# Performance work log

Measured on AMD Instinct MI355X. Metric: run time of the kernel, lower is better.

## Reference

```python
import jax, jax.numpy as jnp
import numpy as np

B, C, H, W, P, D, NH = 16, 3, 512, 512, 16, 128, 4
GH, GW = H // P, W // P
NP_ = GH * GW            # 1024 total patches
PD = C * P * P           # 768 patch dim
NV = NP_ // 4            # 256 visible tokens (mask_ratio = 0.75)
ENC_L, DEC_L = 6, 2
FF = 4 * D

def layer_norm(x, w, b, eps=1e-5):
    m = jnp.mean(x, -1, keepdims=True)
    v = jnp.mean((x - m) ** 2, -1, keepdims=True)
    return (x - m) * jax.lax.rsqrt(v + eps) * w + b

def mha(x, qkv_w, qkv_b, out_w, out_b):
    Bq, S, Dm = x.shape
    hd = Dm // NH
    q, k, v = jnp.split(x @ qkv_w.T + qkv_b, 3, axis=-1)
    sh = lambda t: t.reshape(Bq, S, NH, hd).transpose(0, 2, 1, 3)
    q, k, v = sh(q), sh(k), sh(v)
    scale = jnp.asarray(1.0 / np.sqrt(hd), x.dtype)
    att = jax.nn.softmax(jnp.einsum('bhqd,bhkd->bhqk', q, k) * scale, axis=-1)
    o = jnp.einsum('bhqk,bhkd->bhqd', att, v).transpose(0, 2, 1, 3).reshape(Bq, S, Dm)
    return o @ out_w.T + out_b

def stack(x, qkv_w, qkv_b, out_w, out_b, ln1_w, ln1_b, ff1_w, ff1_b, ff2_w, ff2_b, ln2_w, ln2_b):
    # post-norm nn.TransformerEncoderLayer, eval mode (dropout off), exact gelu
    for i in range(qkv_w.shape[0]):
        x = layer_norm(x + mha(x, qkv_w[i], qkv_b[i], out_w[i], out_b[i]), ln1_w[i], ln1_b[i])
        h = jax.nn.gelu(x @ ff1_w[i].T + ff1_b[i], approximate=False) @ ff2_w[i].T + ff2_b[i]
        x = layer_norm(x + h, ln2_w[i], ln2_b[i])
    return x

def setup_inputs():
    key = jax.random.key(0)
    ks = iter(jax.random.split(key, 64))
    f = lambda *s: jax.random.normal(next(ks), s, jnp.float32) * 0.02
    inp = {
        'x': jax.random.normal(next(ks), (B, C, H, W), jnp.float32),
        'vis_idx': jax.vmap(lambda k: jax.random.permutation(k, NP_))(jax.random.split(next(ks), B))[:, :NV].astype(jnp.int32),
        'w_patch': f(D, PD), 'b_patch': jnp.zeros((D,), jnp.float32),
        'mask_token': f(1, D), 'pos_embed': f(1, NP_, D),
        'w_recon': f(PD, D), 'b_recon': jnp.zeros((PD,), jnp.float32),
    }
    for pre, L in (('enc', ENC_L), ('dec', DEC_L)):
        inp[pre + '_qkv_w'] = f(L, 3 * D, D)
        inp[pre + '_qkv_b'] = jnp.zeros((L, 3 * D), jnp.float32)
        inp[pre + '_out_w'] = f(L, D, D)
        inp[pre + '_out_b'] = jnp.zeros((L, D), jnp.float32)
        inp[pre + '_ln1_w'] = jnp.ones((L, D), jnp.float32)
        inp[pre + '_ln1_b'] = jnp.zeros((L, D), jnp.float32)
        inp[pre + '_ff1_w'] = f(L, FF, D)
        inp[pre + '_ff1_b'] = jnp.zeros((L, FF), jnp.float32)
        inp[pre + '_ff2_w'] = f(L, D, FF)
        inp[pre + '_ff2_b'] = jnp.zeros((L, D), jnp.float32)
        inp[pre + '_ln2_w'] = jnp.ones((L, D), jnp.float32)
        inp[pre + '_ln2_b'] = jnp.zeros((L, D), jnp.float32)
    return inp

def reference(x, vis_idx, w_patch, b_patch, mask_token, pos_embed, w_recon, b_recon,
              enc_qkv_w, enc_qkv_b, enc_out_w, enc_out_b, enc_ln1_w, enc_ln1_b,
              enc_ff1_w, enc_ff1_b, enc_ff2_w, enc_ff2_b, enc_ln2_w, enc_ln2_b,
              dec_qkv_w, dec_qkv_b, dec_out_w, dec_out_b, dec_ln1_w, dec_ln1_b,
              dec_ff1_w, dec_ff1_b, dec_ff2_w, dec_ff2_b, dec_ln2_w, dec_ln2_b):
    # patchify: matches nn.Unfold(kernel=stride=P) channel-major patch layout
    patches = x.reshape(B, C, GH, P, GW, P).transpose(0, 2, 4, 1, 3, 5).reshape(B, NP_, PD)
    tok = patches @ w_patch.T + b_patch                    # [B, NP, D]
    bidx = jnp.arange(B)[:, None]
    vis = tok[bidx, vis_idx]                               # [B, NV, D] packed visible tokens
    enc = stack(vis, enc_qkv_w, enc_qkv_b, enc_out_w, enc_out_b, enc_ln1_w, enc_ln1_b,
                enc_ff1_w, enc_ff1_b, enc_ff2_w, enc_ff2_b, enc_ln2_w, enc_ln2_b)
    # mask_token everywhere, scatter encoded tokens back to their positions
    full = jnp.broadcast_to(mask_token, (B, NP_, D)).at[bidx, vis_idx].set(enc)
    full = full + pos_embed
    dec = stack(full, dec_qkv_w, dec_qkv_b, dec_out_w, dec_out_b, dec_ln1_w, dec_ln1_b,
                dec_ff1_w, dec_ff1_b, dec_ff2_w, dec_ff2_b, dec_ln2_w, dec_ln2_b)
    rec = dec @ w_recon.T + b_recon                        # [B, NP, PD]
    # unpatchify: [B,GH,GW,C,P,P] -> permute(0,3,1,4,2,5) -> [B,C,H,W]
    img = rec.reshape(B, GH, GW, C, P, P).transpose(0, 3, 1, 4, 2, 5).reshape(B, C, H, W)
    return img
```

## Files before the change

kernel.cpp:

```cpp
#include <hip/hip_runtime.h>
#include <math.h>

typedef unsigned short ushort_t;
typedef __attribute__((ext_vector_type(8))) short bf16x8;
typedef __attribute__((ext_vector_type(4))) float f32x4;
typedef __attribute__((ext_vector_type(16))) float f32x16;
typedef __attribute__((ext_vector_type(2))) unsigned uint2v;

__device__ __forceinline__ ushort_t f2bf(float f){
  union{float f; unsigned u;} v; v.f = f;
  unsigned r = v.u + 0x7FFFu + ((v.u >> 16) & 1u);
  return (ushort_t)(r >> 16);
}
__device__ __forceinline__ float bf2f(ushort_t h){
  union{unsigned u; float f;} v; v.u = ((unsigned)h) << 16; return v.f;
}
__device__ __forceinline__ float erf_fast(float x){
  float ax = fabsf(x);
  float t = 1.f / fmaf(0.3275911f, ax, 1.f);
  float y = t*fmaf(t, fmaf(t, fmaf(t, fmaf(t, 1.061405429f, -1.453152027f),
            1.421413741f), -0.284496736f), 0.254829592f);
  float r = 1.f - y * __expf(-ax*ax);
  return copysignf(r, x);
}
__device__ __forceinline__ float gelu_fast(float v){
  return 0.5f * v * (1.f + erf_fast(v * 0.70710678118654752f));
}
#define GLD16(gp, lp) __builtin_amdgcn_global_load_lds( \
    (const __attribute__((address_space(1))) void*)(gp), \
    (__attribute__((address_space(3))) void*)(lp), 16, 0, 0)

static __device__ __forceinline__ f32x4 mfma16(bf16x8 a, bf16x8 b, f32x4 c){
  return __builtin_amdgcn_mfma_f32_16x16x32_bf16(a, b, c, 0, 0, 0);
}
static __device__ __forceinline__ f32x16 mfma32(bf16x8 a, bf16x8 b, f32x16 c){
  return __builtin_amdgcn_mfma_f32_32x32x16_bf16(a, b, c, 0, 0, 0);
}

template<int BT, int MI, int SRC, int EPI>
__global__ __launch_bounds__(256) void mfma_gemm(
    const ushort_t* __restrict__ A, const ushort_t* __restrict__ W,
    const float* __restrict__ bias, void* __restrict__ Cout,
    int M, int N, int K, ushort_t* __restrict__ vT, int slog, float qs)
{
  __shared__ ushort_t smem[BT*64 + BT*64];
  ushort_t* Al = smem;
  ushort_t* Wl = smem + BT*64;
  const int tid = threadIdx.x;
  const int lane = tid & 63, w = tid >> 6;
  const int wr = w >> 1, wc = w & 1;
  const int g = lane >> 4, lq = lane & 15;
  const int m0 = blockIdx.y * BT, n0 = blockIdx.x * BT;

  const f32x4 zf = {0.f, 0.f, 0.f, 0.f};
  f32x4 acc[MI][MI];
#pragma unroll
  for (int i = 0; i < MI; ++i)
#pragma unroll
    for (int j = 0; j < MI; ++j) acc[i][j] = zf;

  float bv[MI];
#pragma unroll
  for (int ni = 0; ni < MI; ++ni) bv[ni] = bias[n0 + wc*(BT/2) + ni*16 + lq];

  const int KT = K >> 6;
  for (int kt = 0; kt < KT; ++kt) {
    if (kt) __syncthreads();
    const int k0 = kt << 6;
#pragma unroll
    for (int i = 0; i < BT/32; ++i) {
      int chunk = i*256 + tid;
      int row = chunk >> 3, c = chunk & 7;
      int kk = k0 + ((c ^ (row & 7)) << 3);
      const ushort_t* src;
      if (SRC == 0) {
        src = A + (size_t)(m0 + row) * K + kk;
      } else {
        int gm = m0 + row;
        int bb = gm >> 10, pp = gm & 1023, gh = pp >> 5, gw = pp & 31;
        int ci = kk >> 8, rem = kk & 255, py = rem >> 4, px = rem & 15;
        src = A + ((size_t)((bb*3 + ci)*512 + gh*16 + py) * 512 + gw*16 + px);
      }
      GLD16(src, (char*)Al + chunk*16);
    }
#pragma unroll
    for (int i = 0; i < BT/32; ++i) {
      int chunk = i*256 + tid;
      int row = chunk >> 3, c = chunk & 7;
      int kk = k0 + ((c ^ (row & 7)) << 3);
      GLD16(W + (size_t)(n0 + row) * K + kk, (char*)Wl + chunk*16);
    }
    __syncthreads();
#pragma unroll
    for (int ks = 0; ks < 2; ++ks) {
      bf16x8 af[MI], bfr[MI];
#pragma unroll
      for (int mi = 0; mi < MI; ++mi) {
        int row = wr*(BT/2) + mi*16 + lq;
        int c = (ks*4 + g) ^ (row & 7);
        af[mi] = *(const bf16x8*)((const char*)Al + row*128 + c*16);
      }
#pragma unroll
      for (int ni = 0; ni < MI; ++ni) {
        int row = wc*(BT/2) + ni*16 + lq;
        int c = (ks*4 + g) ^ (row & 7);
        bfr[ni] = *(const bf16x8*)((const char*)Wl + row*128 + c*16);
      }
#pragma unroll
      for (int mi = 0; mi < MI; ++mi)
#pragma unroll
        for (int ni = 0; ni < MI; ++ni)
          acc[mi][ni] = mfma16(af[mi], bfr[ni], acc[mi][ni]);
    }
  }

  if (EPI == 3 && n0 >= 256) {
    const int Sm1 = (1 << slog) - 1;
#pragma unroll
    for (int mi = 0; mi < MI; ++mi) {
      int gm0 = m0 + wr*(BT/2) + mi*16 + g*4;
      int bb = gm0 >> slog, s0 = gm0 & Sm1;
#pragma unroll
      for (int ni = 0; ni < MI; ++ni) {
        int n = n0 + wc*(BT/2) + ni*16 + lq;
        int vcol = n - 256, hh = vcol >> 5, dd = vcol & 31;
        unsigned pw0 = ((unsigned)f2bf(acc[mi][ni][0] + bv[ni])) |
                       (((unsigned)f2bf(acc[mi][ni][1] + bv[ni])) << 16);
        unsigned pw1 = ((unsigned)f2bf(acc[mi][ni][2] + bv[ni])) |
                       (((unsigned)f2bf(acc[mi][ni][3] + bv[ni])) << 16);
        uint2 pk; pk.x = pw0; pk.y = pw1;
        *(uint2*)(vT + (((size_t)(bb*4 + hh)*32 + dd) << slog) + s0) = pk;
      }
    }
    return;
  }

  if (EPI == 2) {
    float* img = (float*)Cout;
#pragma unroll
    for (int mi = 0; mi < MI; ++mi) {
#pragma unroll
      for (int r = 0; r < 4; ++r) {
        int gm = m0 + wr*(BT/2) + mi*16 + g*4 + r;
        int bb = gm >> 10, pp = gm & 1023, gh = pp >> 5, gw = pp & 31;
#pragma unroll
        for (int ni = 0; ni < MI; ++ni) {
          int n = n0 + wc*(BT/2) + ni*16 + lq;
          int ci = n >> 8, rem = n & 255, py = rem >> 4, px = rem & 15;
          img[(size_t)((bb*3 + ci)*512 + gh*16 + py)*512 + gw*16 + px] =
              acc[mi][ni][r] + bv[ni];
        }
      }
    }
  } else {
    const float cs = (EPI == 3 && n0 < 128) ? qs : 1.0f;
    __syncthreads();
    constexpr int CPR = BT/8;
#pragma unroll
    for (int mi = 0; mi < MI; ++mi)
#pragma unroll
      for (int ni = 0; ni < MI; ++ni)
#pragma unroll
        for (int r = 0; r < 4; ++r) {
          int row = wr*(BT/2) + mi*16 + g*4 + r;
          int col = wc*(BT/2) + ni*16 + lq;
          float v = acc[mi][ni][r] + bv[ni];
          if (EPI == 3) v *= cs;
          int cc = (col >> 3) ^ (row & (CPR-1));
          smem[row*BT + cc*8 + (col & 7)] = f2bf(v);
        }
    __syncthreads();
    ushort_t* Co = (ushort_t*)Cout;
#pragma unroll
    for (int i = 0; i < BT*BT/2048; ++i) {
      int chunk = i*256 + tid;
      int row = chunk / CPR, cc = chunk % CPR;
      int c = cc ^ (row & (CPR-1));
      bf16x8 v = *(const bf16x8*)((const char*)smem + chunk*16);
      *(bf16x8*)(Co + (size_t)(m0+row)*N + n0 + c*8) = v;
    }
  }
}

template<int MI2, int QKV>
__global__ __launch_bounds__(512, 4) void mega8(
    const ushort_t* __restrict__ Ao, const ushort_t* __restrict__ Wo,
    const float* __restrict__ bo, ushort_t* __restrict__ X,
    const float* __restrict__ l1w, const float* __restrict__ l1b,
    const ushort_t* __restrict__ W1, const float* __restrict__ b1,
    const ushort_t* __restrict__ W2, const float* __restrict__ b2,
    const float* __restrict__ l2w, const float* __restrict__ l2b,
    const ushort_t* __restrict__ Wq, const float* __restrict__ bq,
    ushort_t* __restrict__ qkvb, ushort_t* __restrict__ vT,
    int slog, float qs)
{
  constexpr int BM = MI2 * 16;
  constexpr int TB = BM * 128;
  __shared__ __align__(16) ushort_t Xl[2*BM*64];
  __shared__ __align__(16) ushort_t Hl[8*BM*64];
  __shared__ __align__(16) float red[2][BM][8];
  const int tid = threadIdx.x, lane = tid & 63, w = tid >> 6;
  const int g = lane >> 4, lq = lane & 15;
  const int m0 = blockIdx.x * BM;
  const int col0 = w*16 + lq;
  const f32x4 zf = {0.f,0.f,0.f,0.f};

  f32x4 acc[MI2];
#pragma unroll
  for (int mi = 0; mi < MI2; ++mi) acc[mi] = zf;
  {
    bf16x8 a1[MI2][4], bo8[4];
#pragma unroll
    for (int mi = 0; mi < MI2; ++mi)
#pragma unroll
      for (int kf = 0; kf < 4; ++kf)
        a1[mi][kf] = *(const bf16x8*)(Ao + (size_t)(m0 + mi*16 + lq)*128 + kf*32 + g*8);
#pragma unroll
    for (int kf = 0; kf < 4; ++kf)
      bo8[kf] = *(const bf16x8*)(Wo + (size_t)col0*128 + kf*32 + g*8);
#pragma unroll
    for (int kf = 0; kf < 4; ++kf)
#pragma unroll
      for (int mi = 0; mi < MI2; ++mi)
        acc[mi] = mfma16(a1[mi][kf], bo8[kf], acc[mi]);
  }

  float xp[MI2][4];
  {
    const float bv = bo[col0], lwv = l1w[col0], lbv = l1b[col0];
#pragma unroll
    for (int mi = 0; mi < MI2; ++mi)
#pragma unroll
      for (int r = 0; r < 4; ++r) {
        int row = m0 + mi*16 + g*4 + r;
        float v = acc[mi][r] + bv + bf2f(X[(size_t)row*128 + col0]);
        xp[mi][r] = v;
        float s = v, q = v*v;
        s += __shfl_xor(s,1); s += __shfl_xor(s,2); s += __shfl_xor(s,4); s += __shfl_xor(s,8);
        q += __shfl_xor(q,1); q += __shfl_xor(q,2); q += __shfl_xor(q,4); q += __shfl_xor(q,8);
        if (lq == 0) { red[0][mi*16+g*4+r][w] = s; red[1][mi*16+g*4+r][w] = q; }
      }
    __syncthreads();
#pragma unroll
    for (int mi = 0; mi < MI2; ++mi)
#pragma unroll
      for (int r = 0; r < 4; ++r) {
        int rl = mi*16 + g*4 + r;
        float4 s0 = *(const float4*)&red[0][rl][0], s1 = *(const float4*)&red[0][rl][4];
        float4 q0 = *(const float4*)&red[1][rl][0], q1 = *(const float4*)&red[1][rl][4];
        float s = s0.x+s0.y+s0.z+s0.w + s1.x+s1.y+s1.z+s1.w;
        float q = q0.x+q0.y+q0.z+q0.w + q1.x+q1.y+q1.z+q1.w;
        float mean = s * 0.0078125f;
        float var = q * 0.0078125f - mean*mean;
        float rstd = rsqrtf(var + 1e-5f);
        float val = (xp[mi][r]-mean)*rstd*lwv + lbv;
        xp[mi][r] = val;
        int kt = col0 >> 6, c8 = (col0 & 63) >> 3, he = col0 & 7;
        *(ushort_t*)((char*)Xl + kt*TB + rl*128 + ((c8 ^ (rl & 7)) << 4) + he*2) = f2bf(val);
      }
  }
  __syncthreads();

  bf16x8 a2[MI2][4];
#pragma unroll
  for (int mi = 0; mi < MI2; ++mi)
#pragma unroll
    for (int kf = 0; kf < 4; ++kf) {
      int kt = kf >> 1, row = mi*16 + lq;
      int c = ((kf & 1)*4 + g) ^ (row & 7);
      a2[mi][kf] = *(const bf16x8*)((const char*)Xl + kt*TB + row*128 + c*16);
    }

#pragma unroll
  for (int hp = 0; hp < 4; ++hp) {
    const int hid = hp*128 + col0;
    bf16x8 b18[4];
#pragma unroll
    for (int kf = 0; kf < 4; ++kf)
      b18[kf] = *(const bf16x8*)(W1 + (size_t)hid*128 + kf*32 + g*8);
    f32x4 acc1[MI2];
#pragma unroll
    for (int mi = 0; mi < MI2; ++mi) acc1[mi] = zf;
#pragma unroll
    for (int kf = 0; kf < 4; ++kf)
#pragma unroll
      for (int mi = 0; mi < MI2; ++mi)
        acc1[mi] = mfma16(a2[mi][kf], b18[kf], acc1[mi]);
    const float bb = b1[hid];
    const int hkt = hid >> 6, hc8 = (hid & 63) >> 3, he = hid & 7;
#pragma unroll
    for (int mi = 0; mi < MI2; ++mi)
#pragma unroll
      for (int r = 0; r < 4; ++r) {
        int mrow = mi*16 + g*4 + r;
        float hv = gelu_fast(acc1[mi][r] + bb);
        *(ushort_t*)((char*)Hl + hkt*TB + mrow*128 + ((hc8 ^ (mrow & 7)) << 4) + he*2) = f2bf(hv);
      }
  }
  __syncthreads();

  f32x4 acc2[MI2];
#pragma unroll
  for (int mi = 0; mi < MI2; ++mi) acc2[mi] = zf;
#pragma unroll
  for (int kf = 0; kf < 16; ++kf) {
    int kt = kf >> 1;
    bf16x8 af[MI2], bfr;
#pragma unroll
    for (int mi = 0; mi < MI2; ++mi) {
      int row = mi*16 + lq;
      int c = ((kf & 1)*4 + g) ^ (row & 7);
      af[mi] = *(const bf16x8*)((const char*)Hl + kt*TB + row*128 + c*16);
    }
    bfr = *(const bf16x8*)(W2 + (size_t)col0*512 + kf*32 + g*8);
#pragma unroll
    for (int mi = 0; mi < MI2; ++mi)
      acc2[mi] = mfma16(af[mi], bfr, acc2[mi]);
  }

  {
    const float bv = b2[col0], lwv = l2w[col0], lbv = l2b[col0];
#pragma unroll
    for (int mi = 0; mi < MI2; ++mi)
#pragma unroll
      for (int r = 0; r < 4; ++r) {
        float v = acc2[mi][r] + bv + xp[mi][r];
        xp[mi][r] = v;
        float s = v, q = v*v;
        s += __shfl_xor(s,1); s += __shfl_xor(s,2); s += __shfl_xor(s,4); s += __shfl_xor(s,8);
        q += __shfl_xor(q,1); q += __shfl_xor(q,2); q += __shfl_xor(q,4); q += __shfl_xor(q,8);
        if (lq == 0) { red[0][mi*16+g*4+r][w] = s; red[1][mi*16+g*4+r][w] = q; }
      }
    __syncthreads();
#pragma unroll
    for (int mi = 0; mi < MI2; ++mi)
#pragma unroll
      for (int r = 0; r < 4; ++r) {
        int rl = mi*16 + g*4 + r;
        float4 s0 = *(const float4*)&red[0][rl][0], s1 = *(const float4*)&red[0][rl][4];
        float4 q0 = *(const float4*)&red[1][rl][0], q1 = *(const float4*)&red[1][rl][4];
        float s = s0.x+s0.y+s0.z+s0.w + s1.x+s1.y+s1.z+s1.w;
        float q = q0.x+q0.y+q0.z+q0.w + q1.x+q1.y+q1.z+q1.w;
        float mean = s * 0.0078125f;
        float var = q * 0.0078125f - mean*mean;
        float rstd = rsqrtf(var + 1e-5f);
        float val = (xp[mi][r]-mean)*rstd*lwv + lbv;
        ushort_t hv = f2bf(val);
        X[(size_t)(m0+rl)*128 + col0] = hv;
        if (QKV) {
          int kt = col0 >> 6, c8 = (col0 & 63) >> 3, he = col0 & 7;
          *(ushort_t*)((char*)Xl + kt*TB + rl*128 + ((c8 ^ (rl & 7)) << 4) + he*2) = hv;
        }
      }
  }

  if (QKV) {
    __syncthreads();
    bf16x8 a3[MI2][4];
#pragma unroll
    for (int mi = 0; mi < MI2; ++mi)
#pragma unroll
      for (int kf = 0; kf < 4; ++kf) {
        int kt = kf >> 1, row = mi*16 + lq;
        int c = ((kf & 1)*4 + g) ^ (row & 7);
        a3[mi][kf] = *(const bf16x8*)((const char*)Xl + kt*TB + row*128 + c*16);
      }
    const int Sm1 = (1 << slog) - 1;
#pragma unroll
    for (int pp = 0; pp < 3; ++pp) {
      const int colq = pp*128 + col0;
      bf16x8 bq8[4];
#pragma unroll
      for (int kf = 0; kf < 4; ++kf)
        bq8[kf] = *(const bf16x8*)(Wq + (size_t)colq*128 + kf*32 + g*8);
      f32x4 aq[MI2];
#pragma unroll
      for (int mi = 0; mi < MI2; ++mi) aq[mi] = zf;
#pragma unroll
      for (int kf = 0; kf < 4; ++kf)
#pragma unroll
        for (int mi = 0; mi < MI2; ++mi)
          aq[mi] = mfma16(a3[mi][kf], bq8[kf], aq[mi]);
      const float bias = bq[colq];
      if (pp < 2) {
        const float sc = (pp == 0) ? qs : 1.f;
#pragma unroll
        for (int mi = 0; mi < MI2; ++mi)
#pragma unroll
          for (int r = 0; r < 4; ++r) {
            int row = m0 + mi*16 + g*4 + r;
            qkvb[(size_t)row*384 + colq] = f2bf((aq[mi][r] + bias)*sc);
          }
      } else {
        const int hh = col0 >> 5, dd = col0 & 31;
#pragma unroll
        for (int mi = 0; mi < MI2; ++mi) {
          int gm0 = m0 + mi*16 + g*4;
          int bb = gm0 >> slog, s0 = gm0 & Sm1;
          unsigned pw0 = ((unsigned)f2bf(aq[mi][0] + bias)) |
                         (((unsigned)f2bf(aq[mi][1] + bias)) << 16);
          unsigned pw1 = ((unsigned)f2bf(aq[mi][2] + bias)) |
                         (((unsigned)f2bf(aq[mi][3] + bias)) << 16);
          uint2 pk; pk.x = pw0; pk.y = pw1;
          *(uint2*)(vT + (((size_t)(bb*4 + hh)*32 + dd) << slog) + s0) = pk;
        }
      }
    }
  }
}

template<int S, int NTW>
__global__ __launch_bounds__(256) void attn32s(
    const ushort_t* __restrict__ qkv, const ushort_t* __restrict__ vTg,
    ushort_t* __restrict__ o)
{
  __shared__ __align__(16) char smem[32768];
  const int tid = threadIdx.x, lane = tid & 63, w = tid >> 6;
  const int hi = lane >> 5, lq = lane & 31;
  constexpr int QB = S/32;
  constexpr int NBLK = QB*64;
  int lin = blockIdx.x;
  int nid = (lin & 7)*(NBLK/8) + (lin >> 3);
  int bx = nid % QB, bh = nid / QB;
  int h = bh & 3, b = bh >> 2;
  const int q0 = bx*32;

  bf16x8 bq0 = *(const bf16x8*)(qkv + (size_t)(b*S + q0 + lq)*384 + h*32 + hi*8);
  bf16x8 bq1 = *(const bf16x8*)(qkv + (size_t)(b*S + q0 + lq)*384 + h*32 + 16 + hi*8);

  f32x16 O;
#pragma unroll
  for (int i = 0; i < 16; ++i) O[i] = 0.f;
  const f32x16 z16 = O;
  float l = 0.f;

  char* Kb = smem + w*8192;
  char* Vb = Kb + 4096;

  auto stageK = [&](int j0, int ci){
    int k = ci >> 2, cp = ci & 3, c = cp ^ (k & 3);
    GLD16(qkv + (size_t)(b*S + j0 + k)*384 + 128 + h*32 + c*8, Kb + ci*16);
  };
  auto stageV = [&](int j0, int ci){
    int d = ci >> 3, cp = ci & 7, c = cp ^ (d & 7);
    GLD16(vTg + (size_t)(bh*32 + d)*S + j0 + c*8, Vb + ci*16);
  };
  auto sm_pack = [&](const f32x16& stv, unsigned* wd){
    float p[16];
#pragma unroll
    for (int r = 0; r < 16; ++r) { p[r] = __expf(stv[r]); l += p[r]; }
#pragma unroll
    for (int i = 0; i < 8; ++i) {
      unsigned u0 = __float_as_uint(p[2*i])   + 0x8000u;
      unsigned u1 = __float_as_uint(p[2*i+1]) + 0x8000u;
      wd[i] = (u0 >> 16) | (u1 & 0xFFFF0000u);
    }
  };
  auto pvstep = [&](unsigned* wd, int mt){
    uint2v s02 = __builtin_amdgcn_permlane32_swap(wd[0], wd[2], false, false);
    uint2v s13 = __builtin_amdgcn_permlane32_swap(wd[1], wd[3], false, false);
    uint2v s46 = __builtin_amdgcn_permlane32_swap(wd[4], wd[6], false, false);
    uint2v s57 = __builtin_amdgcn_permlane32_swap(wd[5], wd[7], false, false);
    union { unsigned u[4]; bf16x8 v; } pa0, pa1;
    pa0.u[0] = s02[0]; pa0.u[1] = s13[0]; pa0.u[2] = s02[1]; pa0.u[3] = s13[1];
    pa1.u[0] = s46[0]; pa1.u[1] = s57[0]; pa1.u[2] = s46[1]; pa1.u[3] = s57[1];
    int d = lq;
    bf16x8 v0 = *(const bf16x8*)(Vb + d*128 + (((mt*4 + hi)     ^ (d & 7)) << 4));
    bf16x8 v1 = *(const bf16x8*)(Vb + d*128 + (((mt*4 + 2 + hi) ^ (d & 7)) << 4));
    O = mfma32(pa0.v, v0, O);
    O = mfma32(pa1.v, v1, O);
  };
  auto computeTile = [&](){
    const int k0 = lq, k1 = 32 + lq;
    bf16x8 a00 = *(const bf16x8*)(Kb + k0*64 + (((hi)     ^ (k0 & 3)) << 4));
    bf16x8 a01 = *(const bf16x8*)(Kb + k0*64 + (((2 + hi) ^ (k0 & 3)) << 4));
    f32x16 st0 = mfma32(a00, bq0, z16);
    st0 = mfma32(a01, bq1, st0);
    bf16x8 a10 = *(const bf16x8*)(Kb + k1*64 + (((hi)     ^ (k1 & 3)) << 4));
    bf16x8 a11 = *(const bf16x8*)(Kb + k1*64 + (((2 + hi) ^ (k1 & 3)) << 4));
    f32x16 st1 = mfma32(a10, bq0, z16);
    st1 = mfma32(a11, bq1, st1);
    unsigned wd0[8], wd1[8];
    sm_pack(st0, wd0);
    sm_pack(st1, wd1);
    pvstep(wd0, 0);
    pvstep(wd1, 1);
  };

#pragma unroll
  for (int i = 0; i < NTW; ++i) {
    const int j0 = (w + 4*i)*64;
#pragma unroll
    for (int c = 0; c < 4; ++c) stageK(j0, c*64 + lane);
#pragma unroll
    for (int c = 0; c < 4; ++c) stageV(j0, c*64 + lane);
    asm volatile("s_waitcnt vmcnt(0)" ::: "memory");
    __builtin_amdgcn_sched_barrier(0);
    computeTile();
    asm volatile("" ::: "memory");
  }

  float lw = l + __shfl_xor(l, 32);
  __syncthreads();
  float* F = (float*)smem;
#pragma unroll
  for (int r = 0; r < 16; ++r) F[(w*16 + r)*64 + lane] = O[r];
  if (hi == 0) F[4096 + w*32 + lq] = lw;
  __syncthreads();
  if (w == 0) {
    float lt = F[4096 + lq] + F[4096 + 32 + lq] + F[4096 + 64 + lq] + F[4096 + 96 + lq];
    float linv = 1.f / lt;
#pragma unroll
    for (int r = 0; r < 16; ++r) {
      float s = F[r*64 + lane] + F[(16 + r)*64 + lane] +
                F[(32 + r)*64 + lane] + F[(48 + r)*64 + lane];
      int qr = (r & 3) + 8*(r >> 2) + 4*hi;
      float li = __shfl(linv, qr);
      o[(size_t)(b*S + q0 + qr)*128 + h*32 + lq] = f2bf(s*li);
    }
  }
}

struct CastArgs {
  const float* src[11];
  ushort_t* dst[11];
  int start[11];
};
__global__ __launch_bounds__(256) void cast_all(CastArgs a, int total8){
  int i = blockIdx.x*256 + threadIdx.x;
  if (i >= total8) return;
  int s = 0;
#pragma unroll
  for (int k = 1; k < 11; ++k) if (i >= a.start[k]) s = k;
  int off = (i - a.start[s]) * 8;
  const float* sp = a.src[s] + off;
  float4 f0 = *(const float4*)sp;
  float4 f1 = *(const float4*)(sp + 4);
  bf16x8 r;
  r[0]=(short)f2bf(f0.x); r[1]=(short)f2bf(f0.y); r[2]=(short)f2bf(f0.z); r[3]=(short)f2bf(f0.w);
  r[4]=(short)f2bf(f1.x); r[5]=(short)f2bf(f1.y); r[6]=(short)f2bf(f1.z); r[7]=(short)f2bf(f1.w);
  *(bf16x8*)(a.dst[s] + off) = r;
}

__global__ __launch_bounds__(256) void gather_k(const ushort_t* __restrict__ tok,
    const int* __restrict__ vis, ushort_t* __restrict__ xe){
  int i = blockIdx.x*256 + threadIdx.x;
  int r = i >> 4, e = (i & 15)*8;
  int b = r >> 8;
  int p = vis[r];
  *(bf16x8*)(xe + (size_t)r*128 + e) = *(const bf16x8*)(tok + ((size_t)b*1024 + p)*128 + e);
}

__global__ __launch_bounds__(256) void fill_k(const float* __restrict__ mask_tok,
    const float* __restrict__ pos, ushort_t* __restrict__ full){
  int i = blockIdx.x*256 + threadIdx.x;
  int off0 = i*8;
  int d = off0 & 127;
  int p = (off0 >> 7) & 1023;
  float4 m0 = *(const float4*)(mask_tok + d);
  float4 m1 = *(const float4*)(mask_tok + d + 4);
  const float* pp = pos + (size_t)p*128 + d;
  float4 p0 = *(const float4*)pp, p1 = *(const float4*)(pp + 4);
  bf16x8 r;
  r[0]=(short)f2bf(m0.x+p0.x); r[1]=(short)f2bf(m0.y+p0.y);
  r[2]=(short)f2bf(m0.z+p0.z); r[3]=(short)f2bf(m0.w+p0.w);
  r[4]=(short)f2bf(m1.x+p1.x); r[5]=(short)f2bf(m1.y+p1.y);
  r[6]=(short)f2bf(m1.z+p1.z); r[7]=(short)f2bf(m1.w+p1.w);
  *(bf16x8*)(full + off0) = r;
}

__global__ __launch_bounds__(256) void scatter_k(const ushort_t* __restrict__ enc,
    const int* __restrict__ vis, const float* __restrict__ pos, ushort_t* __restrict__ full){
  int i = blockIdx.x*256 + threadIdx.x;
  int r = i >> 4, e = (i & 15)*8;
  int b = r >> 8;
  int p = vis[r];
  bf16x8 ev = *(const bf16x8*)(enc + (size_t)r*128 + e);
  const float* pp = pos + (size_t)p*128 + e;
  float4 p0 = *(const float4*)pp, p1 = *(const float4*)(pp + 4);
  bf16x8 out;
  out[0]=(short)f2bf(bf2f((ushort_t)ev[0]) + p0.x);
  out[1]=(short)f2bf(bf2f((ushort_t)ev[1]) + p0.y);
  out[2]=(short)f2bf(bf2f((ushort_t)ev[2]) + p0.z);
  out[3]=(short)f2bf(bf2f((ushort_t)ev[3]) + p0.w);
  out[4]=(short)f2bf(bf2f((ushort_t)ev[4]) + p1.x);
  out[5]=(short)f2bf(bf2f((ushort_t)ev[5]) + p1.y);
  out[6]=(short)f2bf(bf2f((ushort_t)ev[6]) + p1.z);
  out[7]=(short)f2bf(bf2f((ushort_t)ev[7]) + p1.w);
  *(bf16x8*)(full + ((size_t)b*1024 + p)*128 + e) = out;
}

extern "C" void kernel_launch(void* const* d_in, const int* in_sizes, int n_in,
                              void* d_out, int out_size, void* d_ws, size_t ws_size,
                              hipStream_t stream)
{
  const float* x        = (const float*)d_in[0];
  const int*   vis      = (const int*)d_in[1];
  const float* b_patch  = (const float*)d_in[3];
  const float* mask_tok = (const float*)d_in[4];
  const float* pos      = (const float*)d_in[5];
  const float* b_recon  = (const float*)d_in[7];
  float* out = (float*)d_out;
  const float QS = 0.17677669529663687f;

  ushort_t* ws    = (ushort_t*)d_ws;
  ushort_t* tok   = ws;
  ushort_t* xe    = tok  + 2097152;
  ushort_t* qkvb  = xe   + 524288;
  ushort_t* obuf  = qkvb + 8388608;
  ushort_t* tbuf  = obuf + 2097152;
  ushort_t* xbf   = tbuf + 2097152;
  ushort_t* wbf   = xbf  + 12582912;

  ushort_t* w_qkv_e = wbf;
  ushort_t* w_out_e = w_qkv_e + 294912;
  ushort_t* w_ff1_e = w_out_e + 98304;
  ushort_t* w_ff2_e = w_ff1_e + 393216;
  ushort_t* w_qkv_d = w_ff2_e + 393216;
  ushort_t* w_out_d = w_qkv_d + 98304;
  ushort_t* w_ff1_d = w_out_d + 32768;
  ushort_t* w_ff2_d = w_ff1_d + 131072;
  ushort_t* w_pat   = w_ff2_d + 131072;
  ushort_t* w_rec   = w_pat   + 98304;
  ushort_t* vT      = w_rec   + 98304;

  CastArgs ca;
  const float* srcs[11] = {x, (const float*)d_in[8], (const float*)d_in[10],
                           (const float*)d_in[14], (const float*)d_in[16],
                           (const float*)d_in[20], (const float*)d_in[22],
                           (const float*)d_in[26], (const float*)d_in[28],
                           (const float*)d_in[2], (const float*)d_in[6]};
  ushort_t* dsts[11] = {xbf, w_qkv_e, w_out_e, w_ff1_e, w_ff2_e,
                        w_qkv_d, w_out_d, w_ff1_d, w_ff2_d, w_pat, w_rec};
  int sizes[11] = {12582912, 294912, 98304, 393216, 393216,
                   98304, 32768, 131072, 131072, 98304, 98304};
  int acc8 = 0;
  for (int k = 0; k < 11; ++k){ ca.src[k]=srcs[k]; ca.dst[k]=dsts[k]; ca.start[k]=acc8; acc8 += sizes[k]/8; }
  cast_all<<<dim3((acc8 + 255)/256), 256, 0, stream>>>(ca, acc8);

  mfma_gemm<64,2,1,0><<<dim3(2,256), 256, 0, stream>>>(xbf, w_pat, b_patch, tok, 16384, 128, 768, nullptr, 0, 1.f);
  gather_k<<<dim3(256), 256, 0, stream>>>(tok, vis, xe);

  mfma_gemm<64,2,0,3><<<dim3(6,64), 256, 0, stream>>>(xe, w_qkv_e, (const float*)d_in[9], qkvb, 4096, 384, 128, vT, 8, QS);
  for (int L = 0; L < 6; ++L) {
    const float* ob  = (const float*)d_in[11] + L*128;
    const float* l1w = (const float*)d_in[12] + L*128;
    const float* l1b = (const float*)d_in[13] + L*128;
    const float* f1b = (const float*)d_in[15] + L*512;
    const float* f2b = (const float*)d_in[17] + L*128;
    const float* l2w = (const float*)d_in[18] + L*128;
    const float* l2b = (const float*)d_in[19] + L*128;
    attn32s<256,1><<<dim3(512), 256, 0, stream>>>(qkvb, vT, obuf);
    if (L < 5) {
      mega8<1,1><<<dim3(256), 512, 0, stream>>>(obuf, w_out_e + L*16384, ob, xe,
          l1w, l1b, w_ff1_e + L*65536, f1b, w_ff2_e + L*65536, f2b, l2w, l2b,
          w_qkv_e + (L+1)*49152, (const float*)d_in[9] + (L+1)*384, qkvb, vT, 8, QS);
    } else {
      mega8<1,0><<<dim3(256), 512, 0, stream>>>(obuf, w_out_e + L*16384, ob, xe,
          l1w, l1b, w_ff1_e + L*65536, f1b, w_ff2_e + L*65536, f2b, l2w, l2b,
          w_qkv_e, (const float*)d_in[9], qkvb, vT, 8, QS);
    }
  }

  fill_k<<<dim3(1024), 256, 0, stream>>>(mask_tok, pos, tok);
  scatter_k<<<dim3(256), 256, 0, stream>>>(xe, vis, pos, tok);

  mfma_gemm<128,4,0,3><<<dim3(3,128), 256, 0, stream>>>(tok, w_qkv_d, (const float*)d_in[21], qkvb, 16384, 384, 128, vT, 10, QS);
  for (int L = 0; L < 2; ++L) {
    const float* ob  = (const float*)d_in[23] + L*128;
    const float* l1w = (const float*)d_in[24] + L*128;
    const float* l1b = (const float*)d_in[25] + L*128;
    const float* f1b = (const float*)d_in[27] + L*512;
    const float* f2b = (const float*)d_in[29] + L*128;
    const float* l2w = (const float*)d_in[30] + L*128;
    const float* l2b = (const float*)d_in[31] + L*128;
    attn32s<1024,4><<<dim3(2048), 256, 0, stream>>>(qkvb, vT, obuf);
    if (L < 1) {
      mega8<1,1><<<dim3(1024), 512, 0, stream>>>(obuf, w_out_d + L*16384, ob, tok,
          l1w, l1b, w_ff1_d + L*65536, f1b, w_ff2_d + L*65536, f2b, l2w, l2b,
          w_qkv_d + 49152, (const float*)d_in[21] + 384, qkvb, vT, 10, QS);
    } else {
      mega8<1,0><<<dim3(1024), 512, 0, stream>>>(obuf, w_out_d + L*16384, ob, tok,
          l1w, l1b, w_ff1_d + L*65536, f1b, w_ff2_d + L*65536, f2b, l2w, l2b,
          w_qkv_d, (const float*)d_in[21], qkvb, vT, 10, QS);
    }
  }

  mfma_gemm<128,4,0,2><<<dim3(6,128), 256, 0, stream>>>(tok, w_rec, b_recon, out, 16384, 768, 128, nullptr, 0, 1.f);
}
```

Measured before the change: 362.3 us.

## Replace tiled GEMMs for QKV and reconstruction with register-resident row-block kernels

Adds two new kernels, qkv_mega and recon_mega. They load a small row block of the 128-wide activation into registers and loop over all output columns, reading weight fragments directly from global memory with no LDS staging. These replace the LDS-tiled mfma_gemm for the initial encoder and decoder QKV projections and for the final reconstruction, whose K=128 leaves little reuse for tiling to exploit. The decoder mega8 calls also move to a 32-row block (MI2=2), which halves the grid and doubles per-block work. In exchange, weights are re-read by every block and the QKV stores are scattered 2-byte writes with no smem coalescing.

```diff
diff --git a/kernel.cpp b/kernel.cpp
--- a/kernel.cpp
+++ b/kernel.cpp
@@ -41,7 +41,7 @@
 __global__ __launch_bounds__(256) void mfma_gemm(
     const ushort_t* __restrict__ A, const ushort_t* __restrict__ W,
     const float* __restrict__ bias, void* __restrict__ Cout,
-    int M, int N, int K, ushort_t* __restrict__ vT, int slog, float qs)
+    int M, int N, int K)
 {
   __shared__ ushort_t smem[BT*64 + BT*64];
   ushort_t* Al = smem;
@@ -114,71 +114,140 @@
     }
   }
 
-  if (EPI == 3 && n0 >= 256) {
-    const int Sm1 = (1 << slog) - 1;
-#pragma unroll
-    for (int mi = 0; mi < MI; ++mi) {
-      int gm0 = m0 + wr*(BT/2) + mi*16 + g*4;
-      int bb = gm0 >> slog, s0 = gm0 & Sm1;
-#pragma unroll
-      for (int ni = 0; ni < MI; ++ni) {
-        int n = n0 + wc*(BT/2) + ni*16 + lq;
-        int vcol = n - 256, hh = vcol >> 5, dd = vcol & 31;
-        unsigned pw0 = ((unsigned)f2bf(acc[mi][ni][0] + bv[ni])) |
-                       (((unsigned)f2bf(acc[mi][ni][1] + bv[ni])) << 16);
-        unsigned pw1 = ((unsigned)f2bf(acc[mi][ni][2] + bv[ni])) |
-                       (((unsigned)f2bf(acc[mi][ni][3] + bv[ni])) << 16);
+  __syncthreads();
+  constexpr int CPR = BT/8;
+#pragma unroll
+  for (int mi = 0; mi < MI; ++mi)
+#pragma unroll
+    for (int ni = 0; ni < MI; ++ni)
+#pragma unroll
+      for (int r = 0; r < 4; ++r) {
+        int row = wr*(BT/2) + mi*16 + g*4 + r;
+        int col = wc*(BT/2) + ni*16 + lq;
+        float v = acc[mi][ni][r] + bv[ni];
+        int cc = (col >> 3) ^ (row & (CPR-1));
+        smem[row*BT + cc*8 + (col & 7)] = f2bf(v);
+      }
+  __syncthreads();
+  ushort_t* Co = (ushort_t*)Cout;
+#pragma unroll
+  for (int i = 0; i < BT*BT/2048; ++i) {
+    int chunk = i*256 + tid;
+    int row = chunk / CPR, cc = chunk % CPR;
+    int c = cc ^ (row & (CPR-1));
+    bf16x8 v = *(const bf16x8*)((const char*)smem + chunk*16);
+    *(bf16x8*)(Co + (size_t)(m0+row)*N + n0 + c*8) = v;
+  }
+}
+
+template<int MI2>
+__global__ __launch_bounds__(512, 4) void qkv_mega(
+    const ushort_t* __restrict__ X, const ushort_t* __restrict__ Wq,
+    const float* __restrict__ bq, ushort_t* __restrict__ qkvb,
+    ushort_t* __restrict__ vT, int slog, float qs)
+{
+  constexpr int BM = MI2 * 16;
+  const int tid = threadIdx.x, lane = tid & 63, w = tid >> 6;
+  const int g = lane >> 4, lq = lane & 15;
+  const int m0 = blockIdx.x * BM;
+  const int col0 = w*16 + lq;
+  const f32x4 zf = {0.f,0.f,0.f,0.f};
+
+  bf16x8 a[MI2][4];
+#pragma unroll
+  for (int mi = 0; mi < MI2; ++mi)
+#pragma unroll
+    for (int kf = 0; kf < 4; ++kf)
+      a[mi][kf] = *(const bf16x8*)(X + (size_t)(m0 + mi*16 + lq)*128 + kf*32 + g*8);
+
+  const int Sm1 = (1 << slog) - 1;
+#pragma unroll
+  for (int pp = 0; pp < 3; ++pp) {
+    const int colq = pp*128 + col0;
+    bf16x8 bw[4];
+#pragma unroll
+    for (int kf = 0; kf < 4; ++kf)
+      bw[kf] = *(const bf16x8*)(Wq + (size_t)colq*128 + kf*32 + g*8);
+    f32x4 aq[MI2];
+#pragma unroll
+    for (int mi = 0; mi < MI2; ++mi) aq[mi] = zf;
+#pragma unroll
+    for (int kf = 0; kf < 4; ++kf)
+#pragma unroll
+      for (int mi = 0; mi < MI2; ++mi)
+        aq[mi] = mfma16(a[mi][kf], bw[kf], aq[mi]);
+    const float bias = bq[colq];
+    if (pp < 2) {
+      const float sc = (pp == 0) ? qs : 1.f;
+#pragma unroll
+      for (int mi = 0; mi < MI2; ++mi)
+#pragma unroll
+        for (int r = 0; r < 4; ++r) {
+          int row = m0 + mi*16 + g*4 + r;
+          qkvb[(size_t)row*384 + colq] = f2bf((aq[mi][r] + bias)*sc);
+        }
+    } else {
+      const int hh = col0 >> 5, dd = col0 & 31;
+#pragma unroll
+      for (int mi = 0; mi < MI2; ++mi) {
+        int gm0 = m0 + mi*16 + g*4;
+        int bb = gm0 >> slog, s0 = gm0 & Sm1;
+        unsigned pw0 = ((unsigned)f2bf(aq[mi][0] + bias)) |
+                       (((unsigned)f2bf(aq[mi][1] + bias)) << 16);
+        unsigned pw1 = ((unsigned)f2bf(aq[mi][2] + bias)) |
+                       (((unsigned)f2bf(aq[mi][3] + bias)) << 16);
         uint2 pk; pk.x = pw0; pk.y = pw1;
         *(uint2*)(vT + (((size_t)(bb*4 + hh)*32 + dd) << slog) + s0) = pk;
       }
     }
-    return;
-  }
-
-  if (EPI == 2) {
-    float* img = (float*)Cout;
-#pragma unroll
-    for (int mi = 0; mi < MI; ++mi) {
+  }
+}
+
+template<int MI2>
+__global__ __launch_bounds__(512, 4) void recon_mega(
+    const ushort_t* __restrict__ X, const ushort_t* __restrict__ Wr,
+    const float* __restrict__ br, float* __restrict__ img)
+{
+  constexpr int BM = MI2 * 16;
+  const int tid = threadIdx.x, lane = tid & 63, w = tid >> 6;
+  const int g = lane >> 4, lq = lane & 15;
+  const int m0 = blockIdx.x * BM;
+  const int col0 = w*16 + lq;
+  const f32x4 zf = {0.f,0.f,0.f,0.f};
+
+  bf16x8 a[MI2][4];
+#pragma unroll
+  for (int mi = 0; mi < MI2; ++mi)
+#pragma unroll
+    for (int kf = 0; kf < 4; ++kf)
+      a[mi][kf] = *(const bf16x8*)(X + (size_t)(m0 + mi*16 + lq)*128 + kf*32 + g*8);
+
+#pragma unroll
+  for (int np = 0; np < 6; ++np) {
+    const int col = np*128 + col0;
+    bf16x8 bw[4];
+#pragma unroll
+    for (int kf = 0; kf < 4; ++kf)
+      bw[kf] = *(const bf16x8*)(Wr + (size_t)col*128 + kf*32 + g*8);
+    f32x4 acc[MI2];
+#pragma unroll
+    for (int mi = 0; mi < MI2; ++mi) acc[mi] = zf;
+#pragma unroll
+    for (int kf = 0; kf < 4; ++kf)
+#pragma unroll
+      for (int mi = 0; mi < MI2; ++mi)
+        acc[mi] = mfma16(a[mi][kf], bw[kf], acc[mi]);
+    const float bias = br[col];
+    const int ci = col >> 8, rem = col & 255, py = rem >> 4, px = rem & 15;
+#pragma unroll
+    for (int mi = 0; mi < MI2; ++mi)
 #pragma unroll
       for (int r = 0; r < 4; ++r) {
-        int gm = m0 + wr*(BT/2) + mi*16 + g*4 + r;
-        int bb = gm >> 10, pp = gm & 1023, gh = pp >> 5, gw = pp & 31;
-#pragma unroll
-        for (int ni = 0; ni < MI; ++ni) {
-          int n = n0 + wc*(BT/2) + ni*16 + lq;
-          int ci = n >> 8, rem = n & 255, py = rem >> 4, px = rem & 15;
-          img[(size_t)((bb*3 + ci)*512 + gh*16 + py)*512 + gw*16 + px] =
-              acc[mi][ni][r] + bv[ni];
-        }
-      }
-    }
-  } else {
-    const float cs = (EPI == 3 && n0 < 128) ? qs : 1.0f;
-    __syncthreads();
-    constexpr int CPR = BT/8;
-#pragma unroll
-    for (int mi = 0; mi < MI; ++mi)
-#pragma unroll
-      for (int ni = 0; ni < MI; ++ni)
-#pragma unroll
-        for (int r = 0; r < 4; ++r) {
-          int row = wr*(BT/2) + mi*16 + g*4 + r;
-          int col = wc*(BT/2) + ni*16 + lq;
-          float v = acc[mi][ni][r] + bv[ni];
-          if (EPI == 3) v *= cs;
-          int cc = (col >> 3) ^ (row & (CPR-1));
-          smem[row*BT + cc*8 + (col & 7)] = f2bf(v);
-        }
-    __syncthreads();
-    ushort_t* Co = (ushort_t*)Cout;
-#pragma unroll
-    for (int i = 0; i < BT*BT/2048; ++i) {
-      int chunk = i*256 + tid;
-      int row = chunk / CPR, cc = chunk % CPR;
-      int c = cc ^ (row & (CPR-1));
-      bf16x8 v = *(const bf16x8*)((const char*)smem + chunk*16);
-      *(bf16x8*)(Co + (size_t)(m0+row)*N + n0 + c*8) = v;
-    }
+        int gm = m0 + mi*16 + g*4 + r;
+        int bb = gm >> 10, pq = gm & 1023, gh = pq >> 5, gw = pq & 31;
+        img[(size_t)((bb*3 + ci)*512 + gh*16 + py)*512 + gw*16 + px] =
+            acc[mi][r] + bias;
+      }
   }
 }
 
@@ -638,10 +707,10 @@
   for (int k = 0; k < 11; ++k){ ca.src[k]=srcs[k]; ca.dst[k]=dsts[k]; ca.start[k]=acc8; acc8 += sizes[k]/8; }
   cast_all<<<dim3((acc8 + 255)/256), 256, 0, stream>>>(ca, acc8);
 
-  mfma_gemm<64,2,1,0><<<dim3(2,256), 256, 0, stream>>>(xbf, w_pat, b_patch, tok, 16384, 128, 768, nullptr, 0, 1.f);
+  mfma_gemm<64,2,1,0><<<dim3(2,256), 256, 0, stream>>>(xbf, w_pat, b_patch, tok, 16384, 128, 768);
   gather_k<<<dim3(256), 256, 0, stream>>>(tok, vis, xe);
 
-  mfma_gemm<64,2,0,3><<<dim3(6,64), 256, 0, stream>>>(xe, w_qkv_e, (const float*)d_in[9], qkvb, 4096, 384, 128, vT, 8, QS);
+  qkv_mega<1><<<dim3(256), 512, 0, stream>>>(xe, w_qkv_e, (const float*)d_in[9], qkvb, vT, 8, QS);
   for (int L = 0; L < 6; ++L) {
     const float* ob  = (const float*)d_in[11] + L*128;
     const float* l1w = (const float*)d_in[12] + L*128;
@@ -665,7 +734,7 @@
   fill_k<<<dim3(1024), 256, 0, stream>>>(mask_tok, pos, tok);
   scatter_k<<<dim3(256), 256, 0, stream>>>(xe, vis, pos, tok);
 
-  mfma_gemm<128,4,0,3><<<dim3(3,128), 256, 0, stream>>>(tok, w_qkv_d, (const float*)d_in[21], qkvb, 16384, 384, 128, vT, 10, QS);
+  qkv_mega<2><<<dim3(512), 512, 0, stream>>>(tok, w_qkv_d, (const float*)d_in[21], qkvb, vT, 10, QS);
   for (int L = 0; L < 2; ++L) {
     const float* ob  = (const float*)d_in[23] + L*128;
     const float* l1w = (const float*)d_in[24] + L*128;
@@ -676,15 +745,15 @@
     const float* l2b = (const float*)d_in[31] + L*128;
     attn32s<1024,4><<<dim3(2048), 256, 0, stream>>>(qkvb, vT, obuf);
     if (L < 1) {
-      mega8<1,1><<<dim3(1024), 512, 0, stream>>>(obuf, w_out_d + L*16384, ob, tok,
+      mega8<2,1><<<dim3(512), 512, 0, stream>>>(obuf, w_out_d + L*16384, ob, tok,
           l1w, l1b, w_ff1_d + L*65536, f1b, w_ff2_d + L*65536, f2b, l2w, l2b,
           w_qkv_d + 49152, (const float*)d_in[21] + 384, qkvb, vT, 10, QS);
     } else {
-      mega8<1,0><<<dim3(1024), 512, 0, stream>>>(obuf, w_out_d + L*16384, ob, tok,
+      mega8<2,0><<<dim3(512), 512, 0, stream>>>(obuf, w_out_d + L*16384, ob, tok,
           l1w, l1b, w_ff1_d + L*65536, f1b, w_ff2_d + L*65536, f2b, l2w, l2b,
           w_qkv_d, (const float*)d_in[21], qkvb, vT, 10, QS);
     }
   }
 
-  mfma_gemm<128,4,0,2><<<dim3(6,128), 256, 0, stream>>>(tok, w_rec, b_recon, out, 16384, 768, 128, nullptr, 0, 1.f);
-}
+  recon_mega<2><<<dim3(512), 512, 0, stream>>>(tok, w_rec, b_recon, out);
+}
```

New measurement: 340.5 us. -6.0%, faster.
